# Kernel tuning notes

Measured on AMD Instinct MI355X. Metric: run time of the kernel, lower is better.

Reference implementation:

```python
import jax, jax.numpy as jnp
import numpy as np
import math

NUM_SEGMENTS = 4      # num_bezier_segments
SHARPNESS = 75.0
SAMPLE_RATE = 16      # curve samples per bezier segment


def _control_radians(S):
    # replicates the __init__ control-polygon angle construction
    theta = math.pi * 2 / (4 * S) + math.atan(math.tan(2 * math.pi / (4 * S)) / 3.0)
    r = []
    for i in range(S):
        base = 2 * math.pi / S * i
        r += [base, base + theta, 2 * math.pi / S * (i + 1) - theta]
    return jnp.asarray(np.asarray(r, dtype=np.float32).reshape(S, 3))


def _quat_rotate_inv(q, p):
    # rotate p (...,3) by the conjugate of quaternion q (...,4), wxyz convention
    q = q / jnp.linalg.norm(q, axis=-1, keepdims=True)
    w = q[..., 0:1]
    v = -q[..., 1:4]
    t = 2.0 * jnp.cross(v, p)
    return p + w * t + jnp.cross(v, t)


def _csg_stump(points, primitive_parameters, iw, uw, is_training):
    pp = jnp.swapaxes(primitive_parameters, 1, 2)          # (B,K,P)
    B, K, P = pp.shape
    S, R = NUM_SEGMENTS, SAMPLE_RATE
    quat = pp[:, :, :4]
    trans = pp[:, :, 4:7]
    height = pp[:, :, 7]                                   # (B,K)
    radius = jnp.abs(pp[:, :, 8:8 + 3 * S].reshape(B, K, S, 3))
    wts = jnp.abs(pp[:, :, 8 + 3 * S:8 + 5 * S].reshape(B, K, S, 2))

    rad = _control_radians(S)                              # (S,3)
    cp = jnp.stack([jnp.cos(rad) * radius, jnp.sin(rad) * radius], axis=-1)  # (B,K,S,3,2)

    # closed rational cubic bezier spline: segment s uses cp[s,0..2] and cp[s+1,0]
    P0, P1, P2 = cp[:, :, :, 0], cp[:, :, :, 1], cp[:, :, :, 2]
    P3 = jnp.roll(P0, -1, axis=2)
    t = jnp.arange(R, dtype=pp.dtype) / R                  # (R,) endpoint-free
    b0 = (1 - t) ** 3; b1 = 3 * t * (1 - t) ** 2; b2 = 3 * t ** 2 * (1 - t); b3 = t ** 3
    w1 = wts[..., 0:1]; w2 = wts[..., 1:2]                 # (B,K,S,1)
    num = (b0[:, None] * P0[..., None, :]
           + (b1[:, None] * w1[..., None]) * P1[..., None, :]
           + (b2[:, None] * w2[..., None]) * P2[..., None, :]
           + b3[:, None] * P3[..., None, :])               # (B,K,S,R,2)
    den = b0 + b1 * w1 + b2 * w2 + b3                       # (B,K,S,R)
    curve = (num / den[..., None]).reshape(B, K, S * R, 2)  # (B,K,N,2)

    # transform query points into each primitive's local frame
    p_loc = _quat_rotate_inv(quat[:, None], points[:, :, None, :] - trans[:, None])  # (B,M,K,3)
    pxy = p_loc[..., :2]
    pz = p_loc[..., 2]

    # point-to-curve distances without materializing the (B,M,K,N,2) diff
    p_sq = jnp.sum(pxy * pxy, axis=-1)                      # (B,M,K)
    c_sq = jnp.sum(curve * curve, axis=-1)                  # (B,K,N)
    dots = jnp.einsum('bmkd,bknd->bmkn', pxy, curve)
    d = jnp.sqrt(jnp.maximum(p_sq[..., None] + c_sq[:, None] - 2.0 * dots, 0.0) + 1e-12)
    ud = jnp.min(d, axis=-1)                                # (B,M,K) unsigned 2D distance
    idx = jnp.argmin(d, axis=-1)
    curve_r = jnp.sqrt(c_sq)                                # (B,K,N)
    r_near = jnp.take_along_axis(jnp.broadcast_to(curve_r[:, None], d.shape),
                                 idx[..., None], axis=-1)[..., 0]
    sign = jax.lax.stop_gradient(jnp.where(jnp.sqrt(p_sq) <= r_near, -1.0, 1.0))
    sdf2d = sign * ud

    # extrusion along z
    dz = jnp.abs(pz) - height[:, None, :]
    primitive_sdf = (jnp.minimum(jnp.maximum(sdf2d, dz), 0.0)
                     + jnp.sqrt(jnp.maximum(sdf2d, 0.0) ** 2 + jnp.maximum(dz, 0.0) ** 2 + 1e-12))
    support_distances = ud

    occ = jax.nn.sigmoid(-primitive_sdf * SHARPNESS)        # (B,M,K)

    # soft intersection: bkc,bmk->bmkc selection
    pre_i = iw[:, None] * occ[..., None] + (1.0 - iw)[:, None]    # (B,M,K,C)
    if is_training:
        w = jax.lax.stop_gradient(jax.nn.softmax(pre_i * -40.0, axis=-2))
        inter = jnp.sum(w * pre_i, axis=-2)                 # (B,M,C)
    else:
        inter = jnp.min(pre_i, axis=-2)

    # soft union
    pre_u = uw[:, None, :] * inter                          # (B,M,C)
    if is_training:
        w = jax.lax.stop_gradient(jax.nn.softmax(pre_u * 40.0, axis=-1))
        occupancies = jnp.sum(w * pre_u, axis=-1)           # (B,M)
    else:
        occupancies = jnp.max(pre_u, axis=-1)

    return occupancies, primitive_sdf, inter, support_distances


def setup_inputs() -> dict:
    key = jax.random.key(0)
    k1, k2, k3, k4 = jax.random.split(key, 4)
    B, M, K, C = 4, 8192, 64, 32
    P = 8 + 5 * NUM_SEGMENTS  # 28
    return {
        'sample_point_coordinates': jax.random.uniform(k1, (B, M, 3), dtype=jnp.float32),
        'primitive_parameters': jax.random.normal(k2, (B, P, K), dtype=jnp.float32),
        'intersection_layer_weights': jax.random.uniform(k3, (B, K, C), dtype=jnp.float32),
        'union_layer_weights': jax.random.uniform(k4, (B, C), dtype=jnp.float32),
        'is_training': 1,
    }


def reference(sample_point_coordinates, primitive_parameters, intersection_layer_weights,
              union_layer_weights, is_training):
    return _csg_stump(sample_point_coordinates, primitive_parameters,
                      intersection_layer_weights, union_layer_weights, bool(is_training))
```

## Files before the change

kernel.cpp:

```cpp
#include <hip/hip_runtime.h>
#include <math.h>

#define Bb 4
#define Mm 8192
#define Kk 64
#define Cc 32
#define Pp 28

#define OFF_PSDF  (Bb*Mm)
#define OFF_INTER (Bb*Mm + Bb*Mm*Kk)
#define OFF_SD    (Bb*Mm + Bb*Mm*Kk + Bb*Mm*Cc)

#define W40    57.707801635558535f
#define NL2_40 (-0.017328679513998632f)
#define S75    108.20212806667225f
#define EPS_OCC 1e-6f

struct Rad12 { float v[12]; };

__device__ __forceinline__ float fexp2(float x){ return __builtin_amdgcn_exp2f(x); }
__device__ __forceinline__ float frcp(float x){ return __builtin_amdgcn_rcpf(x); }
__device__ __forceinline__ float bperm(int idx4, float v){
    return __int_as_float(__builtin_amdgcn_ds_bpermute(idx4, __float_as_int(v)));
}

__global__ __launch_bounds__(256)
void curve_prep(const float* __restrict__ pp, const float* __restrict__ iw_g,
                Rad12 rad,
                float* __restrict__ ws_c, float* __restrict__ params_ws,
                float2* __restrict__ st_ws, float4* __restrict__ tbl_ws)
{
    const int g = blockIdx.x * 256 + threadIdx.x;
    const int k = g & 63;
    const int n = (g >> 6) & 63;
    const int b = g >> 12;

#define PP(p) pp[((b * Pp) + (p)) * Kk + k]

    const int s  = n >> 4;
    const int it = n & 15;
    const float t = (float)it * 0.0625f;
    const int s1 = (s + 1) & 3;

    float r0 = fabsf(PP(8 + 3 * s + 0));
    float r1 = fabsf(PP(8 + 3 * s + 1));
    float r2 = fabsf(PP(8 + 3 * s + 2));
    float r3 = fabsf(PP(8 + 3 * s1 + 0));
    float w1 = fabsf(PP(20 + 2 * s + 0));
    float w2 = fabsf(PP(20 + 2 * s + 1));

    float a0 = rad.v[3 * s + 0], a1 = rad.v[3 * s + 1];
    float a2 = rad.v[3 * s + 2], a3 = rad.v[3 * s1 + 0];

    float P0x = cosf(a0) * r0, P0y = sinf(a0) * r0;
    float P1x = cosf(a1) * r1, P1y = sinf(a1) * r1;
    float P2x = cosf(a2) * r2, P2y = sinf(a2) * r2;
    float P3x = cosf(a3) * r3, P3y = sinf(a3) * r3;

    float omt = 1.0f - t;
    float b0 = omt * omt * omt;
    float b1 = (3.0f * t) * (omt * omt);
    float b2 = (3.0f * (t * t)) * omt;
    float b3 = t * t * t;
    float bw1 = b1 * w1, bw2 = b2 * w2;
    float den = ((b0 + bw1) + bw2) + b3;
    float nx  = ((b0 * P0x + bw1 * P1x) + bw2 * P2x) + b3 * P3x;
    float ny  = ((b0 * P0y + bw1 * P1y) + bw2 * P2y) + b3 * P3y;

    float cx = nx / den, cy = ny / den;
    const int j = n >> 1, h = n & 1;
    float* base = ws_c + (((b * 32 + j) * 64) + k) * 4;
    base[h]     = -2.0f * cx;
    base[2 + h] = -2.0f * cy;

    if (n < 8) {
        float val;
        if (n < 4) {
            float q0 = PP(0), q1 = PP(1), q2 = PP(2), q3 = PP(3);
            float nrm = sqrtf(q0 * q0 + q1 * q1 + q2 * q2 + q3 * q3);
            val = PP(n) / nrm;
        } else {
            val = PP(n);
        }
        params_ws[(b * Kk + k) * 8 + n] = val;
    }
#undef PP

    if (n >= 32) {
        const int idx = (n - 32) * 64 + k;
        float w  = iw_g[b * 2048 + idx];
        float a  = w * (-W40);
        float bb = (w - 1.0f) * W40;
        float e0 = fexp2(bb);
        tbl_ws[b * 2048 + idx] = make_float4(a, bb, e0, e0 * bb);
    }

    if (blockIdx.x == 0 && threadIdx.x < 128) {
        const int tb = threadIdx.x >> 5, tc = threadIdx.x & 31;
        float S = 0.0f, T = 0.0f;
        for (int kk = 0; kk < 64; ++kk) {
            float w   = iw_g[tb * 2048 + kk * 32 + tc];
            float b40 = (w - 1.0f) * W40;
            float e   = fexp2(b40);
            S += e;
            T  = fmaf(e, b40, T);
        }
        st_ws[threadIdx.x] = make_float2(S, T);
    }
}

__global__ __launch_bounds__(512)
void csg_main(const float* __restrict__ pts, const float* __restrict__ uw_g,
              const int* __restrict__ flag,
              const float* __restrict__ ws_c, const float* __restrict__ params_ws,
              const float2* __restrict__ st_ws, const float4* __restrict__ tbl_ws,
              float* __restrict__ out)
{
    __shared__ __align__(16) float s_pool[8192];

    const int tid = threadIdx.x;
    const int bid = blockIdx.x;
    const int b   = bid >> 8;
    const int m0  = (bid & 255) << 5;

    {
        const float4* cs = (const float4*)(ws_c + (size_t)b * 8192);
        float4* cd = (float4*)s_pool;
#pragma unroll
        for (int i = 0; i < 4; ++i) cd[tid + i * 512] = cs[tid + i * 512];
    }
    __syncthreads();

    const int wid  = tid >> 6;
    const int lane = tid & 63;
    const int k    = lane;
    const int pt0  = b * Mm + m0 + (wid << 2);

    const float4* prm4 = (const float4*)(params_ws + ((b << 6) + k) * 8);
    float4 q4 = prm4[0];
    float4 t4 = prm4[1];

    const float4* pts4 = (const float4*)(pts + (size_t)pt0 * 3);
    float4 A = pts4[0], Bv = pts4[1], Cv = pts4[2];
    float pxs[4] = {A.x, A.w, Bv.z, Cv.y};
    float pys[4] = {A.y, Bv.x, Bv.w, Cv.z};
    float pzs[4] = {A.z, Bv.y, Cv.x, Cv.w};

    float px4[4], py4[4], plzv[4], psq[4];
    {
        float vx = -q4.y, vy = -q4.z, vz = -q4.w, qw = q4.x;
#pragma unroll
        for (int p = 0; p < 4; ++p) {
            float px = pxs[p] - t4.x, py = pys[p] - t4.y, pz = pzs[p] - t4.z;
            float t1x = 2.0f * (vy * pz - vz * py);
            float t1y = 2.0f * (vz * px - vx * pz);
            float t1z = 2.0f * (vx * py - vy * px);
            float plx = px + qw * t1x + (vy * t1z - vz * t1y);
            float ply = py + qw * t1y + (vz * t1x - vx * t1z);
            plzv[p] = pz + qw * t1z + (vx * t1y - vy * t1x);
            psq[p]  = plx * plx + ply * ply;
            px4[p]  = 4.0f * plx;
            py4[p]  = 4.0f * ply;
        }
    }

    float best4[4] = {1e30f, 1e30f, 1e30f, 1e30f};
    float bcsq4[4] = {0.0f, 0.0f, 0.0f, 0.0f};
    {
        const float4* cdp = (const float4*)&s_pool[k * 4];
#pragma unroll 4
        for (int j = 0; j < 32; ++j) {
            float4 cd = cdp[j * 64];
            float cq4x = fmaf(cd.x, cd.x, cd.z * cd.z);
            float cq4y = fmaf(cd.y, cd.y, cd.w * cd.w);
#pragma unroll
            for (int p = 0; p < 4; ++p) {
                float da = fmaf(cd.x, px4[p], fmaf(cd.z, py4[p], cq4x));
                if (da < best4[p]) { best4[p] = da; bcsq4[p] = cq4x; }
                float db = fmaf(cd.y, px4[p], fmaf(cd.w, py4[p], cq4y));
                if (db < best4[p]) { best4[p] = db; bcsq4[p] = cq4y; }
            }
        }
    }

    float occ[4];
    unsigned long long mu = 0ull;
#pragma unroll
    for (int p = 0; p < 4; ++p) {
        float d2    = psq[p] + 0.25f * best4[p];
        float bq    = 0.25f * bcsq4[p];
        float ud    = sqrtf(fmaxf(d2, 0.0f) + 1e-12f);
        float sgn   = (psq[p] <= bq) ? -1.0f : 1.0f;
        float sdf2d = sgn * ud;
        float dzv   = fabsf(plzv[p]) - t4.w;
        float inner = fminf(fmaxf(sdf2d, dzv), 0.0f);
        float r1m   = fmaxf(sdf2d, 0.0f), r2m = fmaxf(dzv, 0.0f);
        float psdf  = inner + sqrtf(r1m * r1m + r2m * r2m + 1e-12f);
        out[OFF_PSDF + (pt0 + p) * Kk + k] = psdf;
        out[OFF_SD   + (pt0 + p) * Kk + k] = ud;
        occ[p]  = frcp(1.0f + fexp2(S75 * psdf));
        mu |= __ballot(occ[p] > EPS_OCC);
    }

    const int c  = lane & 31;
    const int hi = lane >> 5;
    const int kb = hi << 5;
    float2 s0t0 = st_ws[b * 32 + c];
    const float4* tbl4 = tbl_ws + b * 2048;

    const int training = flag[0];

    float inter[4];
    if (training) {
        float sw[4], swp[4];
#pragma unroll
        for (int p = 0; p < 4; ++p) {
            sw[p]  = hi ? 0.0f : s0t0.x;
            swp[p] = hi ? 0.0f : s0t0.y;
        }
        unsigned long long m = hi ? (mu >> 32) : (mu & 0xFFFFFFFFull);
        while (m) {
            int kk = __builtin_ctzll(m) + kb; m &= m - 1;
            int i4 = kk << 2;
            float o0 = bperm(i4, occ[0]);
            float o1 = bperm(i4, occ[1]);
            float o2 = bperm(i4, occ[2]);
            float o3 = bperm(i4, occ[3]);
            float4 wv = tbl4[kk * 32 + c];
            float os[4] = {o0, o1, o2, o3};
#pragma unroll
            for (int p = 0; p < 4; ++p) {
                float pre = fmaf(wv.x, os[p], wv.y);
                float e   = fexp2(pre);
                sw[p]  += (e - wv.z);
                swp[p] += fmaf(e, pre, -wv.w);
            }
        }
#pragma unroll
        for (int p = 0; p < 4; ++p) {
            float swt  = sw[p]  + __shfl_xor(sw[p], 32, 64);
            float swpt = swp[p] + __shfl_xor(swp[p], 32, 64);
            inter[p] = swpt * frcp(swt) * NL2_40;
        }
    } else {
        float mx[4] = {-1e30f, -1e30f, -1e30f, -1e30f};
#pragma unroll 4
        for (int j = 0; j < 32; ++j) {
            int kk = kb + j;
            int i4 = kk << 2;
            float4 wv = tbl4[kk * 32 + c];
            float os[4] = {bperm(i4, occ[0]), bperm(i4, occ[1]),
                           bperm(i4, occ[2]), bperm(i4, occ[3])};
#pragma unroll
            for (int p = 0; p < 4; ++p)
                mx[p] = fmaxf(mx[p], fmaf(wv.x, os[p], wv.y));
        }
#pragma unroll
        for (int p = 0; p < 4; ++p) {
            float m2 = fmaxf(mx[p], __shfl_xor(mx[p], 32, 64));
            inter[p] = m2 * NL2_40;
        }
    }

    if (lane < Cc) {
#pragma unroll
        for (int p = 0; p < 4; ++p)
            out[OFF_INTER + (pt0 + p) * Cc + c] = inter[p];
    }

    float uwv = uw_g[b * Cc + c];
    float resv[4];
    if (training) {
#pragma unroll
        for (int p = 0; p < 4; ++p) {
            float pu  = uwv * inter[p];
            float e   = fexp2(W40 * pu);
            float num = e * pu, den = e;
#pragma unroll
            for (int msk = 16; msk >= 1; msk >>= 1) {
                num += __shfl_xor(num, msk, 64);
                den += __shfl_xor(den, msk, 64);
            }
            resv[p] = num * frcp(den);
        }
    } else {
#pragma unroll
        for (int p = 0; p < 4; ++p) {
            float pu = uwv * inter[p];
#pragma unroll
            for (int msk = 16; msk >= 1; msk >>= 1)
                pu = fmaxf(pu, __shfl_xor(pu, msk, 64));
            resv[p] = pu;
        }
    }
    if (lane == 0)
        *(float4*)(out + pt0) = make_float4(resv[0], resv[1], resv[2], resv[3]);
}

extern "C" void kernel_launch(void* const* d_in, const int* in_sizes, int n_in,
                              void* d_out, int out_size, void* d_ws, size_t ws_size,
                              hipStream_t stream)
{
    const float* pts  = (const float*)d_in[0];
    const float* pp   = (const float*)d_in[1];
    const float* iw   = (const float*)d_in[2];
    const float* uw   = (const float*)d_in[3];
    const int*   flag = (const int*)d_in[4];
    float* out = (float*)d_out;

    float*  ws_c   = (float*)d_ws;
    float*  params = ws_c + 32768;
    float2* st_ws  = (float2*)(params + 2048);
    float4* tbl_ws = (float4*)((char*)d_ws + 140 * 1024);

    Rad12 rad;
    const double th = M_PI * 2.0 / 16.0 + atan(tan(2.0 * M_PI / 16.0) / 3.0);
    for (int i = 0; i < 4; ++i) {
        double base = 2.0 * M_PI / 4.0 * (double)i;
        rad.v[3 * i + 0] = (float)base;
        rad.v[3 * i + 1] = (float)(base + th);
        rad.v[3 * i + 2] = (float)(2.0 * M_PI / 4.0 * (double)(i + 1) - th);
    }

    curve_prep<<<64, 256, 0, stream>>>(pp, iw, rad, ws_c, params, st_ws, tbl_ws);
    csg_main<<<Bb * Mm / 32, 512, 0, stream>>>(pts, uw, flag,
                                               ws_c, params, st_ws, tbl_ws, out);
}
```

Baseline: 39.68 us.

## Split wave halves by point pair instead of by primitive half in intersection stage

The intersection/union stage now gives each half-wave two of the four points and has it loop over all 64 primitives, instead of each half-wave covering 32 primitives for all four points. This drops the cross-half reductions and halves the per-iteration exp and bpermute work per lane. In exchange, the sparse loop now iterates over the union of active primitives for a point pair (up to 64), which can mean more iterations and more divergence between the halves.

```diff
diff --git a/kernel.cpp b/kernel.cpp
--- a/kernel.cpp
+++ b/kernel.cpp
@@ -184,7 +184,7 @@
     }
 
     float occ[4];
-    unsigned long long mu = 0ull;
+    unsigned long long msk[4];
 #pragma unroll
     for (int p = 0; p < 4; ++p) {
         float d2    = psq[p] + 0.25f * best4[p];
@@ -199,102 +199,86 @@
         out[OFF_PSDF + (pt0 + p) * Kk + k] = psdf;
         out[OFF_SD   + (pt0 + p) * Kk + k] = ud;
         occ[p]  = frcp(1.0f + fexp2(S75 * psdf));
-        mu |= __ballot(occ[p] > EPS_OCC);
+        msk[p]  = __ballot(occ[p] > EPS_OCC);
     }
 
     const int c  = lane & 31;
     const int hi = lane >> 5;
-    const int kb = hi << 5;
     float2 s0t0 = st_ws[b * 32 + c];
     const float4* tbl4 = tbl_ws + b * 2048;
 
+    const int pA = hi << 1, pB = pA + 1;
+    float occA = occ[pA], occB = occ[pB];
+    unsigned long long mpair = msk[pA] | msk[pB];
+
     const int training = flag[0];
 
-    float inter[4];
+    float interA, interB;
     if (training) {
-        float sw[4], swp[4];
-#pragma unroll
-        for (int p = 0; p < 4; ++p) {
-            sw[p]  = hi ? 0.0f : s0t0.x;
-            swp[p] = hi ? 0.0f : s0t0.y;
-        }
-        unsigned long long m = hi ? (mu >> 32) : (mu & 0xFFFFFFFFull);
+        float swA = s0t0.x, swpA = s0t0.y;
+        float swB = s0t0.x, swpB = s0t0.y;
+        unsigned long long m = mpair;
         while (m) {
-            int kk = __builtin_ctzll(m) + kb; m &= m - 1;
+            int kk = __builtin_ctzll(m); m &= m - 1;
             int i4 = kk << 2;
-            float o0 = bperm(i4, occ[0]);
-            float o1 = bperm(i4, occ[1]);
-            float o2 = bperm(i4, occ[2]);
-            float o3 = bperm(i4, occ[3]);
+            float oA = bperm(i4, occA);
+            float oB = bperm(i4, occB);
             float4 wv = tbl4[kk * 32 + c];
-            float os[4] = {o0, o1, o2, o3};
-#pragma unroll
-            for (int p = 0; p < 4; ++p) {
-                float pre = fmaf(wv.x, os[p], wv.y);
-                float e   = fexp2(pre);
-                sw[p]  += (e - wv.z);
-                swp[p] += fmaf(e, pre, -wv.w);
-            }
-        }
-#pragma unroll
-        for (int p = 0; p < 4; ++p) {
-            float swt  = sw[p]  + __shfl_xor(sw[p], 32, 64);
-            float swpt = swp[p] + __shfl_xor(swp[p], 32, 64);
-            inter[p] = swpt * frcp(swt) * NL2_40;
-        }
+            float preA = fmaf(wv.x, oA, wv.y);
+            float preB = fmaf(wv.x, oB, wv.y);
+            float eA = fexp2(preA), eB = fexp2(preB);
+            swA  += (eA - wv.z);
+            swpA += fmaf(eA, preA, -wv.w);
+            swB  += (eB - wv.z);
+            swpB += fmaf(eB, preB, -wv.w);
+        }
+        interA = swpA * frcp(swA) * NL2_40;
+        interB = swpB * frcp(swB) * NL2_40;
     } else {
-        float mx[4] = {-1e30f, -1e30f, -1e30f, -1e30f};
+        float mxA = -1e30f, mxB = -1e30f;
 #pragma unroll 4
-        for (int j = 0; j < 32; ++j) {
-            int kk = kb + j;
+        for (int kk = 0; kk < 64; ++kk) {
             int i4 = kk << 2;
+            float oA = bperm(i4, occA);
+            float oB = bperm(i4, occB);
             float4 wv = tbl4[kk * 32 + c];
-            float os[4] = {bperm(i4, occ[0]), bperm(i4, occ[1]),
-                           bperm(i4, occ[2]), bperm(i4, occ[3])};
-#pragma unroll
-            for (int p = 0; p < 4; ++p)
-                mx[p] = fmaxf(mx[p], fmaf(wv.x, os[p], wv.y));
-        }
-#pragma unroll
-        for (int p = 0; p < 4; ++p) {
-            float m2 = fmaxf(mx[p], __shfl_xor(mx[p], 32, 64));
-            inter[p] = m2 * NL2_40;
-        }
-    }
-
-    if (lane < Cc) {
-#pragma unroll
-        for (int p = 0; p < 4; ++p)
-            out[OFF_INTER + (pt0 + p) * Cc + c] = inter[p];
-    }
+            mxA = fmaxf(mxA, fmaf(wv.x, oA, wv.y));
+            mxB = fmaxf(mxB, fmaf(wv.x, oB, wv.y));
+        }
+        interA = mxA * NL2_40;
+        interB = mxB * NL2_40;
+    }
+
+    out[OFF_INTER + (pt0 + pA) * Cc + c] = interA;
+    out[OFF_INTER + (pt0 + pB) * Cc + c] = interB;
 
     float uwv = uw_g[b * Cc + c];
-    float resv[4];
+    float resA, resB;
     if (training) {
-#pragma unroll
-        for (int p = 0; p < 4; ++p) {
-            float pu  = uwv * inter[p];
-            float e   = fexp2(W40 * pu);
-            float num = e * pu, den = e;
-#pragma unroll
-            for (int msk = 16; msk >= 1; msk >>= 1) {
-                num += __shfl_xor(num, msk, 64);
-                den += __shfl_xor(den, msk, 64);
-            }
-            resv[p] = num * frcp(den);
-        }
+        float puA = uwv * interA, puB = uwv * interB;
+        float eA = fexp2(W40 * puA), eB = fexp2(W40 * puB);
+        float numA = eA * puA, denA = eA;
+        float numB = eB * puB, denB = eB;
+#pragma unroll
+        for (int mk = 16; mk >= 1; mk >>= 1) {
+            numA += __shfl_xor(numA, mk, 64);
+            denA += __shfl_xor(denA, mk, 64);
+            numB += __shfl_xor(numB, mk, 64);
+            denB += __shfl_xor(denB, mk, 64);
+        }
+        resA = numA * frcp(denA);
+        resB = numB * frcp(denB);
     } else {
-#pragma unroll
-        for (int p = 0; p < 4; ++p) {
-            float pu = uwv * inter[p];
-#pragma unroll
-            for (int msk = 16; msk >= 1; msk >>= 1)
-                pu = fmaxf(pu, __shfl_xor(pu, msk, 64));
-            resv[p] = pu;
-        }
-    }
-    if (lane == 0)
-        *(float4*)(out + pt0) = make_float4(resv[0], resv[1], resv[2], resv[3]);
+        float puA = uwv * interA, puB = uwv * interB;
+#pragma unroll
+        for (int mk = 16; mk >= 1; mk >>= 1) {
+            puA = fmaxf(puA, __shfl_xor(puA, mk, 64));
+            puB = fmaxf(puB, __shfl_xor(puB, mk, 64));
+        }
+        resA = puA; resB = puB;
+    }
+    if (c == 0)
+        *(float2*)(out + pt0 + pA) = make_float2(resA, resB);
 }
 
 extern "C" void kernel_launch(void* const* d_in, const int* in_sizes, int n_in,
```

Result: no change. 38.96 us (-1.8%).
